# Kernel tuning notes

Hardware: AMD Instinct MI355X
Metric: run time of the kernel (lower is better)

## Reference

```python
import jax, jax.numpy as jnp
import numpy as np

N_NODES = 100000
D = 128            # node feature dim == hidden_units[0]
N_EDGES = 640000
BN_EPS = 1e-3      # keras BatchNormalization default epsilon


def setup_inputs() -> dict:
    key = jax.random.key(0)
    ks = jax.random.split(key, 12)
    node_repr = jax.random.normal(ks[0], (N_NODES, D), dtype=jnp.float32)
    edges = jax.random.randint(ks[1], (2, N_EDGES), 0, N_NODES, dtype=jnp.int64)
    # ffn_prepare: BN(D) -> Dense(D, gelu)   (dropout inactive at inference)
    bn1_gamma = jax.random.normal(ks[2], (D,), dtype=jnp.float32) * 0.1 + 1.0
    bn1_beta = jax.random.normal(ks[3], (D,), dtype=jnp.float32) * 0.1
    bn1_mean = jax.random.normal(ks[4], (D,), dtype=jnp.float32) * 0.1
    bn1_var = jax.random.uniform(ks[5], (D,), dtype=jnp.float32) + 0.5
    W1 = jax.random.normal(ks[6], (D, D), dtype=jnp.float32) / np.sqrt(D)
    b1 = jnp.zeros((D,), dtype=jnp.float32)
    # update_fn: BN(2D) -> Dense(D, gelu)
    bn2_gamma = jax.random.normal(ks[7], (2 * D,), dtype=jnp.float32) * 0.1 + 1.0
    bn2_beta = jax.random.normal(ks[8], (2 * D,), dtype=jnp.float32) * 0.1
    bn2_mean = jax.random.normal(ks[9], (2 * D,), dtype=jnp.float32) * 0.1
    bn2_var = jax.random.uniform(ks[10], (2 * D,), dtype=jnp.float32) + 0.5
    W2 = jax.random.normal(ks[11], (2 * D, D), dtype=jnp.float32) / np.sqrt(2 * D)
    b2 = jnp.zeros((D,), dtype=jnp.float32)
    return dict(node_repr=node_repr, edges=edges,
                bn1_gamma=bn1_gamma, bn1_beta=bn1_beta, bn1_mean=bn1_mean, bn1_var=bn1_var,
                W1=W1, b1=b1,
                bn2_gamma=bn2_gamma, bn2_beta=bn2_beta, bn2_mean=bn2_mean, bn2_var=bn2_var,
                W2=W2, b2=b2)


def _bn(x, gamma, beta, mean, var):
    # inference-mode batch norm
    return (x - mean) * jax.lax.rsqrt(var + BN_EPS) * gamma + beta


def reference(node_repr, edges, bn1_gamma, bn1_beta, bn1_mean, bn1_var, W1, b1,
              bn2_gamma, bn2_beta, bn2_mean, bn2_var, W2, b2):
    num_nodes = node_repr.shape[0]
    node_indices, neighbour_indices = edges[0], edges[1]
    # gather neighbour features: [E, D]
    neigh = node_repr[neighbour_indices]
    # prepare FFN (BN -> dropout(identity at eval) -> Dense + exact gelu)
    msg = jax.nn.gelu(_bn(neigh, bn1_gamma, bn1_beta, bn1_mean, bn1_var) @ W1 + b1,
                      approximate=False)
    # unsorted_segment_mean: sum / count, empty segments -> 0 (TF semantics)
    sums = jax.ops.segment_sum(msg, node_indices, num_segments=num_nodes)
    cnt = jax.ops.segment_sum(jnp.ones((edges.shape[1],), msg.dtype), node_indices,
                              num_segments=num_nodes)
    agg = sums / jnp.maximum(cnt, 1.0)[:, None]
    # update FFN on concat [node_repr, agg]: [N, 2D] -> [N, D]
    h = jnp.concatenate([node_repr, agg], axis=1)
    out = jax.nn.gelu(_bn(h, bn2_gamma, bn2_beta, bn2_mean, bn2_var) @ W2 + b2,
                      approximate=False)
    return out
```

## Files before the change

kernel.cpp:

```cpp
#include <hip/hip_runtime.h>

#define NN 100000
#define DD 128
#define EE 640000
#define BN_EPS 1e-3f
#define NBLK 391
#define NTILE 6250
#define EPB 1637

typedef __bf16 bf16x8 __attribute__((ext_vector_type(8)));
typedef float f32x4 __attribute__((ext_vector_type(4)));

#define W1F_OFF 0u
#define W2F_OFF 32768u
#define B1F_OFF 98304u
#define B2F_OFF 98816u
#define T_OFF   99328u
#define OFFS_OFF 26099328u
#define ELIST_OFF 26899328u
#define CNTG_OFF ELIST_OFF
#define BOFS_OFF (ELIST_OFF + 611524u)
#define BSUM_OFF 29459328u
#define BOFF_OFF 29461376u
#define AGG_OFF 29464576u

__device__ __forceinline__ float gelu_fast(float x) {
    float x3 = x * x * x;
    float z2 = 1.5957691216057308f * x + 0.07135481627002407f * x3;
    return x / (1.0f + __expf(-z2));
}

__global__ __launch_bounds__(256) void prep_kernel(
    const float* __restrict__ g1, const float* __restrict__ be1,
    const float* __restrict__ m1, const float* __restrict__ v1,
    const float* __restrict__ W1, const float* __restrict__ b1,
    const float* __restrict__ g2, const float* __restrict__ be2,
    const float* __restrict__ m2, const float* __restrict__ v2,
    const float* __restrict__ W2, const float* __restrict__ b2,
    const int* __restrict__ edges,
    __bf16* __restrict__ W1f, __bf16* __restrict__ W2f,
    float* __restrict__ b1f, float* __restrict__ b2f,
    int* __restrict__ cntg)
{
    const int blk = blockIdx.x;
    const int t = threadIdx.x;
    if (blk < 64) {
        const int w = (blk * 256 + t) >> 6;
        const int lane = t & 63;
        if (w < 128) {
            float acc = 0.f;
            for (int k = lane; k < 128; k += 64) {
                float s = g1[k] * rsqrtf(v1[k] + BN_EPS);
                float sh = be1[k] - m1[k] * s;
                acc += sh * W1[k * 128 + w];
            }
#pragma unroll
            for (int off = 32; off > 0; off >>= 1) acc += __shfl_down(acc, off);
            if (lane == 0) b1f[w] = acc + b1[w];
        } else {
            const int n = w - 128;
            float acc = 0.f;
            for (int k = lane; k < 256; k += 64) {
                float s = g2[k] * rsqrtf(v2[k] + BN_EPS);
                float sh = be2[k] - m2[k] * s;
                acc += sh * W2[k * 128 + n];
            }
#pragma unroll
            for (int off = 32; off > 0; off >>= 1) acc += __shfl_down(acc, off);
            if (lane == 0) b2f[n] = acc + b2[n];
        }
    } else if (blk < 256) {
        int tid = (blk - 64) * 256 + t;
        if (tid < 16384) {
            int idx = tid;
            int i = idx & 7, l = (idx >> 3) & 63, nt = (idx >> 9) & 7, kt = idx >> 12;
            int k = kt * 32 + (l >> 4) * 8 + i;
            int n = nt * 16 + (l & 15);
            float s = g1[k] * rsqrtf(v1[k] + BN_EPS);
            W1f[idx] = (__bf16)(s * W1[k * 128 + n]);
        } else {
            int idx = tid - 16384;
            int i = idx & 7, l = (idx >> 3) & 63, nt = (idx >> 9) & 7, kt = idx >> 12;
            int n = nt * 16 + (l & 15);
            int row;
            if (kt < 4) {
                row = kt * 32 + (l >> 4) * 8 + i;
            } else {
                int q = (kt - 4) * 32 + (l >> 4) * 8 + i;
                row = 128 + ((q & 7) * 16 + (q >> 3));
            }
            float s = g2[row] * rsqrtf(v2[row] + BN_EPS);
            W2f[idx] = (__bf16)(s * W2[row * 128 + n]);
        }
    } else {
        __shared__ int cnt[NBLK];
        const int k = blk - 256;
        for (int b = t; b < NBLK; b += 256) cnt[b] = 0;
        __syncthreads();
        const int e0 = k * EPB, e1 = min(e0 + EPB, EE);
        for (int e = e0 + t; e < e1; e += 256)
            atomicAdd(&cnt[edges[e] >> 8], 1);
        __syncthreads();
        for (int b = t; b < NBLK; b += 256) cntg[k * NBLK + b] = cnt[b];
    }
}

__global__ __launch_bounds__(256) void sortb_kernel(const int* __restrict__ cntg,
                                                    int* __restrict__ bofs,
                                                    int* __restrict__ bsum)
{
    const int b = blockIdx.x, t = threadIdx.x;
    __shared__ int sp[256];
    int ia = 2 * t, ib = 2 * t + 1;
    int va = (ia < NBLK) ? cntg[ia * NBLK + b] : 0;
    int vb = (ib < NBLK) ? cntg[ib * NBLK + b] : 0;
    sp[t] = va + vb;
    __syncthreads();
    for (int off = 1; off < 256; off <<= 1) {
        int tmp = (t >= off) ? sp[t - off] : 0;
        __syncthreads();
        sp[t] += tmp;
        __syncthreads();
    }
    int pexcl = sp[t] - (va + vb);
    if (ia < NBLK) bofs[b * NBLK + ia] = pexcl;
    if (ib < NBLK) bofs[b * NBLK + ib] = pexcl + va;
    if (t == 255) bsum[b] = sp[255];
}

__global__ __launch_bounds__(512) void scan_top_kernel(const int* __restrict__ bsum,
                                                       int* __restrict__ boff)
{
    __shared__ int s[512];
    const int t = threadIdx.x;
    int v = (t < NBLK) ? bsum[t] : 0;
    s[t] = v;
    __syncthreads();
    for (int off = 1; off < 512; off <<= 1) {
        int tmp = (t >= off) ? s[t - off] : 0;
        __syncthreads();
        s[t] += tmp;
        __syncthreads();
    }
    if (t < NBLK) boff[t] = s[t] - v;
}

__global__ __launch_bounds__(256) void sortc_ffn1_kernel(
    const int* __restrict__ edges, const int* __restrict__ boff,
    const int* __restrict__ bofs, int* __restrict__ pairbuf,
    const float* __restrict__ X, const __bf16* __restrict__ W1f,
    const float* __restrict__ b1f, __bf16* __restrict__ T)
{
    __shared__ __bf16 sW[16384];
    const int t = threadIdx.x;
    if (blockIdx.x < NBLK) {
        int* cur = (int*)sW;
        const int k = blockIdx.x;
        for (int b = t; b < NBLK; b += 256)
            cur[b] = boff[b] + bofs[b * NBLK + k];
        __syncthreads();
        const int e0 = k * EPB, e1 = min(e0 + EPB, EE);
        for (int e = e0 + t; e < e1; e += 256) {
            int dst = edges[e];
            int src = edges[EE + e];
            int pos = atomicAdd(&cur[dst >> 8], 1);
            pairbuf[pos] = (src << 8) | (dst & 255);
        }
        return;
    }
#pragma unroll
    for (int i = 0; i < 8; ++i) {
        int ch = i * 256 + t;
        *(bf16x8*)(sW + ch * 8) = *(const bf16x8*)(W1f + (size_t)ch * 8);
    }
    __syncthreads();

    const int wave = t >> 6;
    const int lane = t & 63;
    const int c = lane & 15, kh = lane >> 4;
    const int tbase = (blockIdx.x - NBLK) * 8;

    float bias[8];
#pragma unroll
    for (int nt = 0; nt < 8; ++nt) bias[nt] = b1f[nt * 16 + c];

#pragma unroll
    for (int s = 0; s < 2; ++s) {
        const int tile = tbase + s * 4 + wave;
        if (tile >= NTILE) break;
        const float* xr = X + (size_t)(tile * 16 + c) * DD + kh * 8;
        f32x4 r0[4], r1[4];
#pragma unroll
        for (int q = 0; q < 4; ++q) {
            r0[q] = *(const f32x4*)(xr + q * 32);
            r1[q] = *(const f32x4*)(xr + q * 32 + 4);
        }
        bf16x8 af[4];
#pragma unroll
        for (int kt = 0; kt < 4; ++kt) {
            bf16x8 fa;
#pragma unroll
            for (int i = 0; i < 4; ++i) { fa[i] = (__bf16)r0[kt][i]; fa[4 + i] = (__bf16)r1[kt][i]; }
            af[kt] = fa;
        }
        f32x4 acc[8] = {};
#pragma unroll
        for (int kt = 0; kt < 4; ++kt)
#pragma unroll
            for (int nt = 0; nt < 8; ++nt) {
                bf16x8 bfr = *(const bf16x8*)(sW + ((kt * 8 + nt) * 64 + lane) * 8);
                acc[nt] = __builtin_amdgcn_mfma_f32_16x16x32_bf16(af[kt], bfr, acc[nt], 0, 0, 0);
            }
#pragma unroll
        for (int r = 0; r < 4; ++r) {
            int row = tile * 16 + kh * 4 + r;
            bf16x8 o;
#pragma unroll
            for (int nt = 0; nt < 8; ++nt)
                o[nt] = (__bf16)gelu_fast(acc[nt][r] + bias[nt]);
            *(bf16x8*)(T + (size_t)row * DD + c * 8) = o;
        }
    }
}

__global__ __launch_bounds__(256) void p2_kernel(const int* __restrict__ boff,
                                                 const int* __restrict__ pairbuf,
                                                 int* __restrict__ elist,
                                                 int* __restrict__ offs)
{
    __shared__ int s[256];
    __shared__ int cur[256];
    const int b = blockIdx.x, t = threadIdx.x;
    const int start = boff[b];
    const int end = (b + 1 < NBLK) ? boff[b + 1] : EE;
    cur[t] = 0;
    __syncthreads();
    for (int e = start + t; e < end; e += 256)
        atomicAdd(&cur[pairbuf[e] & 255], 1);
    __syncthreads();
    int v = cur[t];
    s[t] = v;
    __syncthreads();
    for (int off = 1; off < 256; off <<= 1) {
        int tmp = (t >= off) ? s[t - off] : 0;
        __syncthreads();
        s[t] += tmp;
        __syncthreads();
    }
    int ex = s[t] - v + start;
    const int node = b * 256 + t;
    if (node <= NN) offs[node] = ex;
    __syncthreads();
    cur[t] = ex;
    __syncthreads();
    for (int e = start + t; e < end; e += 256) {
        int item = pairbuf[e];
        int pos = atomicAdd(&cur[item & 255], 1);
        elist[pos] = item >> 8;
    }
}

__global__ __launch_bounds__(256) void agg_kernel(
    const __bf16* __restrict__ T, const int* __restrict__ offs,
    const int* __restrict__ elist, __bf16* __restrict__ Agg)
{
    int t = blockIdx.x * 256 + threadIdx.x;
    int node = t >> 4, j = t & 15;
    if (node >= NN) return;
    const int lane = threadIdx.x & 63;
    const int gbase = lane & 48;
    const int beg = offs[node];
    const int end = offs[node + 1];
    const int d = end - beg;
    float acc[8] = {};
    for (int eb = beg; eb < end; eb += 16) {
        int me = eb + (lane & 15);
        int sv = (me < end) ? elist[me] : 0;
        int cnt = min(end - eb, 16);
        int i = 0;
        for (; i + 3 < cnt; i += 4) {
            int s0 = __shfl(sv, gbase + i);
            int s1 = __shfl(sv, gbase + i + 1);
            int s2 = __shfl(sv, gbase + i + 2);
            int s3 = __shfl(sv, gbase + i + 3);
            bf16x8 v0 = *(const bf16x8*)(T + (size_t)s0 * DD + j * 8);
            bf16x8 v1 = *(const bf16x8*)(T + (size_t)s1 * DD + j * 8);
            bf16x8 v2 = *(const bf16x8*)(T + (size_t)s2 * DD + j * 8);
            bf16x8 v3 = *(const bf16x8*)(T + (size_t)s3 * DD + j * 8);
#pragma unroll
            for (int q = 0; q < 8; ++q)
                acc[q] += ((float)v0[q] + (float)v1[q]) + ((float)v2[q] + (float)v3[q]);
        }
        for (; i < cnt; ++i) {
            int s0 = __shfl(sv, gbase + i);
            bf16x8 v0 = *(const bf16x8*)(T + (size_t)s0 * DD + j * 8);
#pragma unroll
            for (int q = 0; q < 8; ++q) acc[q] += (float)v0[q];
        }
    }
    const float inv = 1.0f / fmaxf((float)d, 1.0f);
    bf16x8 o;
#pragma unroll
    for (int q = 0; q < 8; ++q) o[q] = (__bf16)(acc[q] * inv);
    *(bf16x8*)(Agg + (size_t)node * DD + j * 8) = o;
}

__global__ __launch_bounds__(256) void ffn2_kernel(
    const float* __restrict__ X, const __bf16* __restrict__ Agg,
    const __bf16* __restrict__ W2f, const float* __restrict__ b2f,
    float* __restrict__ out)
{
    const int wave = threadIdx.x >> 6;
    const int lane = threadIdx.x & 63;
    const int unit = blockIdx.x * 4 + wave;
    const int tile = unit >> 1;
    const int h = unit & 1;
    if (tile >= NTILE) return;
    const int c = lane & 15, kh = lane >> 4;

    const int rowA = tile * 16 + c;
    const float* xr = X + (size_t)rowA * DD + kh * 8;
    const __bf16* ar = Agg + (size_t)rowA * DD + kh * 8;

    f32x4 r0[4], r1[4];
    bf16x8 ag[4];
#pragma unroll
    for (int q = 0; q < 4; ++q) {
        r0[q] = *(const f32x4*)(xr + q * 32);
        r1[q] = *(const f32x4*)(xr + q * 32 + 4);
        ag[q] = *(const bf16x8*)(ar + q * 32);
    }
    bf16x8 bp[4], bq[4];
#pragma unroll
    for (int nt = 0; nt < 4; ++nt)
        bp[nt] = *(const bf16x8*)(W2f + ((size_t)((h * 4 + nt) * 64 + lane)) * 8);

    bf16x8 a[8];
#pragma unroll
    for (int kt = 0; kt < 4; ++kt) {
        bf16x8 fa;
#pragma unroll
        for (int i = 0; i < 4; ++i) { fa[i] = (__bf16)r0[kt][i]; fa[4 + i] = (__bf16)r1[kt][i]; }
        a[kt] = fa;
        a[4 + kt] = ag[kt];
    }

    f32x4 acc[4] = {};
#pragma unroll
    for (int kt = 0; kt < 8; ++kt) {
        if (kt + 1 < 8) {
#pragma unroll
            for (int nt = 0; nt < 4; ++nt) {
                bf16x8 v = *(const bf16x8*)(W2f + ((size_t)(((kt + 1) * 8 + h * 4 + nt) * 64 + lane)) * 8);
                if (kt & 1) bp[nt] = v; else bq[nt] = v;
            }
        }
#pragma unroll
        for (int nt = 0; nt < 4; ++nt) {
            bf16x8 cur = (kt & 1) ? bq[nt] : bp[nt];
            acc[nt] = __builtin_amdgcn_mfma_f32_16x16x32_bf16(a[kt], cur, acc[nt], 0, 0, 0);
        }
    }

    float bias[4];
#pragma unroll
    for (int nt = 0; nt < 4; ++nt) bias[nt] = b2f[(h * 4 + nt) * 16 + c];

#pragma unroll
    for (int r = 0; r < 4; ++r) {
        int row = tile * 16 + kh * 4 + r;
#pragma unroll
        for (int nt = 0; nt < 4; ++nt)
            out[(size_t)row * DD + (h * 4 + nt) * 16 + c] = gelu_fast(acc[nt][r] + bias[nt]);
    }
}

extern "C" void kernel_launch(void* const* d_in, const int* in_sizes, int n_in,
                              void* d_out, int out_size, void* d_ws, size_t ws_size,
                              hipStream_t stream) {
    const float* node_repr = (const float*)d_in[0];
    const int*   edges     = (const int*)d_in[1];
    const float* g1 = (const float*)d_in[2];
    const float* be1 = (const float*)d_in[3];
    const float* m1 = (const float*)d_in[4];
    const float* v1 = (const float*)d_in[5];
    const float* W1 = (const float*)d_in[6];
    const float* b1 = (const float*)d_in[7];
    const float* g2 = (const float*)d_in[8];
    const float* be2 = (const float*)d_in[9];
    const float* m2 = (const float*)d_in[10];
    const float* v2 = (const float*)d_in[11];
    const float* W2 = (const float*)d_in[12];
    const float* b2 = (const float*)d_in[13];

    char* ws = (char*)d_ws;
    __bf16* W1f = (__bf16*)(ws + W1F_OFF);
    __bf16* W2f = (__bf16*)(ws + W2F_OFF);
    float* b1f = (float*)(ws + B1F_OFF);
    float* b2f = (float*)(ws + B2F_OFF);
    __bf16* T  = (__bf16*)(ws + T_OFF);
    int* offs  = (int*)(ws + OFFS_OFF);
    int* elist = (int*)(ws + ELIST_OFF);
    int* cntg  = (int*)(ws + CNTG_OFF);
    int* bofs  = (int*)(ws + BOFS_OFF);
    int* bsum  = (int*)(ws + BSUM_OFF);
    int* boff  = (int*)(ws + BOFF_OFF);
    __bf16* Agg = (__bf16*)(ws + AGG_OFF);
    int* pairbuf = (int*)(ws + AGG_OFF);
    float* out = (float*)d_out;

    hipLaunchKernelGGL(prep_kernel, dim3(256 + NBLK), dim3(256), 0, stream,
                       g1, be1, m1, v1, W1, b1, g2, be2, m2, v2, W2, b2,
                       edges, W1f, W2f, b1f, b2f, cntg);

    hipLaunchKernelGGL(sortb_kernel, dim3(NBLK), dim3(256), 0, stream, cntg, bofs, bsum);
    hipLaunchKernelGGL(scan_top_kernel, dim3(1), dim3(512), 0, stream, bsum, boff);

    hipLaunchKernelGGL(sortc_ffn1_kernel, dim3(NBLK + (NTILE + 7) / 8), dim3(256), 0, stream,
                       edges, boff, bofs, pairbuf, node_repr, W1f, b1f, T);

    hipLaunchKernelGGL(p2_kernel, dim3(NBLK), dim3(256), 0, stream,
                       boff, pairbuf, elist, offs);

    hipLaunchKernelGGL(agg_kernel, dim3((NN * 16 + 255) / 256), dim3(256), 0, stream,
                       T, offs, elist, Agg);

    hipLaunchKernelGGL(ffn2_kernel, dim3((NTILE * 2 + 3) / 4), dim3(256), 0, stream,
                       node_repr, Agg, W2f, b2f, out);
}
```

Before: 110.7 us.

## Cache bf16 node features in FFN1 and make FFN2 persistent with register-held weights

FFN1 now writes a bf16 copy of node features alongside its existing work. FFN2 reads that half-size copy instead of the fp32 input. FFN2 becomes a persistent grid-stride kernel with 768 blocks. Each wave keeps its W2 column slice in registers for the whole run and double-buffers the next tile's loads while computing the current one. This targets FFN2's X read traffic and its per-tile weight reloads, at the cost of an extra 25.6MB write in FFN1 and higher register pressure in FFN2.

```diff
diff --git a/kernel.cpp b/kernel.cpp
--- a/kernel.cpp
+++ b/kernel.cpp
@@ -7,6 +7,7 @@
 #define NBLK 391
 #define NTILE 6250
 #define EPB 1637
+#define FFN2_BLKS 768
 
 typedef __bf16 bf16x8 __attribute__((ext_vector_type(8)));
 typedef float f32x4 __attribute__((ext_vector_type(4)));
@@ -23,6 +24,7 @@
 #define BSUM_OFF 29459328u
 #define BOFF_OFF 29461376u
 #define AGG_OFF 29464576u
+#define XB_OFF  55064576u
 
 __device__ __forceinline__ float gelu_fast(float x) {
     float x3 = x * x * x;
@@ -149,7 +151,8 @@
     const int* __restrict__ edges, const int* __restrict__ boff,
     const int* __restrict__ bofs, int* __restrict__ pairbuf,
     const float* __restrict__ X, const __bf16* __restrict__ W1f,
-    const float* __restrict__ b1f, __bf16* __restrict__ T)
+    const float* __restrict__ b1f, __bf16* __restrict__ T,
+    __bf16* __restrict__ Xb)
 {
     __shared__ __bf16 sW[16384];
     const int t = threadIdx.x;
@@ -188,7 +191,8 @@
     for (int s = 0; s < 2; ++s) {
         const int tile = tbase + s * 4 + wave;
         if (tile >= NTILE) break;
-        const float* xr = X + (size_t)(tile * 16 + c) * DD + kh * 8;
+        const size_t rowb = (size_t)(tile * 16 + c) * DD;
+        const float* xr = X + rowb + kh * 8;
         f32x4 r0[4], r1[4];
 #pragma unroll
         for (int q = 0; q < 4; ++q) {
@@ -203,6 +207,10 @@
             for (int i = 0; i < 4; ++i) { fa[i] = (__bf16)r0[kt][i]; fa[4 + i] = (__bf16)r1[kt][i]; }
             af[kt] = fa;
         }
+#pragma unroll
+        for (int kt = 0; kt < 4; ++kt)
+            *(bf16x8*)(Xb + rowb + kt * 32 + kh * 8) = af[kt];
+
         f32x4 acc[8] = {};
 #pragma unroll
         for (int kt = 0; kt < 4; ++kt)
@@ -305,73 +313,70 @@
     *(bf16x8*)(Agg + (size_t)node * DD + j * 8) = o;
 }
 
+#define FFN2_LOAD(TT, XA, GA)                                              \
+    {                                                                      \
+        const size_t rb = (size_t)((TT) * 16 + c) * DD + kh * 8;           \
+        _Pragma("unroll")                                                  \
+        for (int q = 0; q < 4; ++q) {                                      \
+            XA[q] = *(const bf16x8*)(Xb + rb + q * 32);                    \
+            GA[q] = *(const bf16x8*)(Agg + rb + q * 32);                   \
+        }                                                                  \
+    }
+
+#define FFN2_COMP(TT, XA, GA)                                              \
+    {                                                                      \
+        f32x4 acc0 = {}, acc1 = {};                                        \
+        _Pragma("unroll")                                                  \
+        for (int kt = 0; kt < 4; ++kt) {                                   \
+            acc0 = __builtin_amdgcn_mfma_f32_16x16x32_bf16(XA[kt], Bf[kt][0], acc0, 0, 0, 0); \
+            acc1 = __builtin_amdgcn_mfma_f32_16x16x32_bf16(XA[kt], Bf[kt][1], acc1, 0, 0, 0); \
+        }                                                                  \
+        _Pragma("unroll")                                                  \
+        for (int kt = 0; kt < 4; ++kt) {                                   \
+            acc0 = __builtin_amdgcn_mfma_f32_16x16x32_bf16(GA[kt], Bf[4 + kt][0], acc0, 0, 0, 0); \
+            acc1 = __builtin_amdgcn_mfma_f32_16x16x32_bf16(GA[kt], Bf[4 + kt][1], acc1, 0, 0, 0); \
+        }                                                                  \
+        _Pragma("unroll")                                                  \
+        for (int r = 0; r < 4; ++r) {                                      \
+            int row = (TT) * 16 + kh * 4 + r;                              \
+            out[(size_t)row * DD + (w * 2) * 16 + c] = gelu_fast(acc0[r] + bias0); \
+            out[(size_t)row * DD + (w * 2 + 1) * 16 + c] = gelu_fast(acc1[r] + bias1); \
+        }                                                                  \
+    }
+
 __global__ __launch_bounds__(256) void ffn2_kernel(
-    const float* __restrict__ X, const __bf16* __restrict__ Agg,
+    const __bf16* __restrict__ Xb, const __bf16* __restrict__ Agg,
     const __bf16* __restrict__ W2f, const float* __restrict__ b2f,
     float* __restrict__ out)
 {
-    const int wave = threadIdx.x >> 6;
+    const int w = threadIdx.x >> 6;
     const int lane = threadIdx.x & 63;
-    const int unit = blockIdx.x * 4 + wave;
-    const int tile = unit >> 1;
-    const int h = unit & 1;
+    const int c = lane & 15, kh = lane >> 4;
+    const int G = gridDim.x;
+
+    bf16x8 Bf[8][2];
+#pragma unroll
+    for (int kt = 0; kt < 8; ++kt) {
+        Bf[kt][0] = *(const bf16x8*)(W2f + ((size_t)((kt * 8 + w * 2) * 64 + lane)) * 8);
+        Bf[kt][1] = *(const bf16x8*)(W2f + ((size_t)((kt * 8 + w * 2 + 1) * 64 + lane)) * 8);
+    }
+    const float bias0 = b2f[(w * 2) * 16 + c];
+    const float bias1 = b2f[(w * 2 + 1) * 16 + c];
+
+    int tile = blockIdx.x;
     if (tile >= NTILE) return;
-    const int c = lane & 15, kh = lane >> 4;
-
-    const int rowA = tile * 16 + c;
-    const float* xr = X + (size_t)rowA * DD + kh * 8;
-    const __bf16* ar = Agg + (size_t)rowA * DD + kh * 8;
-
-    f32x4 r0[4], r1[4];
-    bf16x8 ag[4];
-#pragma unroll
-    for (int q = 0; q < 4; ++q) {
-        r0[q] = *(const f32x4*)(xr + q * 32);
-        r1[q] = *(const f32x4*)(xr + q * 32 + 4);
-        ag[q] = *(const bf16x8*)(ar + q * 32);
-    }
-    bf16x8 bp[4], bq[4];
-#pragma unroll
-    for (int nt = 0; nt < 4; ++nt)
-        bp[nt] = *(const bf16x8*)(W2f + ((size_t)((h * 4 + nt) * 64 + lane)) * 8);
-
-    bf16x8 a[8];
-#pragma unroll
-    for (int kt = 0; kt < 4; ++kt) {
-        bf16x8 fa;
-#pragma unroll
-        for (int i = 0; i < 4; ++i) { fa[i] = (__bf16)r0[kt][i]; fa[4 + i] = (__bf16)r1[kt][i]; }
-        a[kt] = fa;
-        a[4 + kt] = ag[kt];
-    }
-
-    f32x4 acc[4] = {};
-#pragma unroll
-    for (int kt = 0; kt < 8; ++kt) {
-        if (kt + 1 < 8) {
-#pragma unroll
-            for (int nt = 0; nt < 4; ++nt) {
-                bf16x8 v = *(const bf16x8*)(W2f + ((size_t)(((kt + 1) * 8 + h * 4 + nt) * 64 + lane)) * 8);
-                if (kt & 1) bp[nt] = v; else bq[nt] = v;
-            }
-        }
-#pragma unroll
-        for (int nt = 0; nt < 4; ++nt) {
-            bf16x8 cur = (kt & 1) ? bq[nt] : bp[nt];
-            acc[nt] = __builtin_amdgcn_mfma_f32_16x16x32_bf16(a[kt], cur, acc[nt], 0, 0, 0);
-        }
-    }
-
-    float bias[4];
-#pragma unroll
-    for (int nt = 0; nt < 4; ++nt) bias[nt] = b2f[(h * 4 + nt) * 16 + c];
-
-#pragma unroll
-    for (int r = 0; r < 4; ++r) {
-        int row = tile * 16 + kh * 4 + r;
-#pragma unroll
-        for (int nt = 0; nt < 4; ++nt)
-            out[(size_t)row * DD + (h * 4 + nt) * 16 + c] = gelu_fast(acc[nt][r] + bias[nt]);
+    bf16x8 xa[4], ga[4], xb2[4], gb[4];
+    FFN2_LOAD(tile, xa, ga);
+    while (true) {
+        int t2 = tile + G;
+        if (t2 < NTILE) FFN2_LOAD(t2, xb2, gb);
+        FFN2_COMP(tile, xa, ga);
+        if (t2 >= NTILE) break;
+        int t3 = t2 + G;
+        if (t3 < NTILE) FFN2_LOAD(t3, xa, ga);
+        FFN2_COMP(t2, xb2, gb);
+        if (t3 >= NTILE) break;
+        tile = t3;
     }
 }
 
@@ -407,6 +412,7 @@
     int* boff  = (int*)(ws + BOFF_OFF);
     __bf16* Agg = (__bf16*)(ws + AGG_OFF);
     int* pairbuf = (int*)(ws + AGG_OFF);
+    __bf16* Xb = (__bf16*)(ws + XB_OFF);
     float* out = (float*)d_out;
 
     hipLaunchKernelGGL(prep_kernel, dim3(256 + NBLK), dim3(256), 0, stream,
@@ -417,7 +423,7 @@
     hipLaunchKernelGGL(scan_top_kernel, dim3(1), dim3(512), 0, stream, bsum, boff);
 
     hipLaunchKernelGGL(sortc_ffn1_kernel, dim3(NBLK + (NTILE + 7) / 8), dim3(256), 0, stream,
-                       edges, boff, bofs, pairbuf, node_repr, W1f, b1f, T);
+                       edges, boff, bofs, pairbuf, node_repr, W1f, b1f, T, Xb);
 
     hipLaunchKernelGGL(p2_kernel, dim3(NBLK), dim3(256), 0, stream,
                        boff, pairbuf, elist, offs);
@@ -425,6 +431,6 @@
     hipLaunchKernelGGL(agg_kernel, dim3((NN * 16 + 255) / 256), dim3(256), 0, stream,
                        T, offs, elist, Agg);
 
-    hipLaunchKernelGGL(ffn2_kernel, dim3((NTILE * 2 + 3) / 4), dim3(256), 0, stream,
-                       node_repr, Agg, W2f, b2f, out);
-}
+    hipLaunchKernelGGL(ffn2_kernel, dim3(FFN2_BLKS), dim3(256), 0, stream,
+                       Xb, Agg, W2f, b2f, out);
+}
```

Result: faster. 106.7 us (-3.6%).
